# Kernel optimization log

Measured on AMD Instinct MI355X. Metric: run time of the kernel, lower is better.

The kernel has to match this reference:

```python
import jax, jax.numpy as jnp
import numpy as np

N_NODES = 100000
N_EDGES = 1600000
IN_CH = 128
HEADS = 4
OUT_CH = 32


def setup_inputs() -> dict:
    key = jax.random.key(0)
    k = jax.random.split(key, 6)
    x = jax.random.normal(k[0], (N_NODES, IN_CH), dtype=jnp.float32)
    edge_index = jax.random.randint(k[1], (2, N_EDGES), 0, N_NODES, dtype=jnp.int64)
    edge_weight = jax.random.uniform(k[2], (N_EDGES,), dtype=jnp.float32)
    # torch Linear weight layout: (out_features, in_features) = (heads*out_ch, in_ch)
    W = jax.random.normal(k[3], (HEADS * OUT_CH, IN_CH), dtype=jnp.float32) * (1.0 / np.sqrt(IN_CH))
    a_src = jax.random.normal(k[4], (1, HEADS, OUT_CH), dtype=jnp.float32) * 0.1
    a_dst = jax.random.normal(k[5], (1, HEADS, OUT_CH), dtype=jnp.float32) * 0.1
    return {"x": x, "edge_index": edge_index, "edge_weight": edge_weight,
            "W": W, "a_src": a_src, "a_dst": a_dst}


def reference(x, edge_index, edge_weight, W, a_src, a_dst):
    N = x.shape[0]
    H, C = a_src.shape[1], a_src.shape[2]
    # linear projection then reshape to (N, H, C)
    h = (x @ W.T).reshape(N, H, C)
    src, dst = edge_index[0], edge_index[1]
    # per-node attention logits (node-level, then gathered -> same math as
    # (h[src]*a_src).sum(-1), computed once per node instead of per edge)
    s_src = jnp.sum(h * a_src, axis=-1)  # (N, H)
    s_dst = jnp.sum(h * a_dst, axis=-1)  # (N, H)
    alpha = jax.nn.leaky_relu(s_src[src] + s_dst[dst], negative_slope=0.2)  # (E, H)
    alpha = alpha * edge_weight[:, None]
    # segment softmax over dst; torch scatter_reduce amax with include_self=True
    # includes the zero init, so max is taken vs. 0 via zeros init
    amax = jnp.zeros((N, H), dtype=alpha.dtype).at[dst].max(alpha)
    alpha = jnp.exp(alpha - amax[dst])
    asum = jnp.zeros((N, H), dtype=alpha.dtype).at[dst].add(alpha)
    alpha = alpha / (asum[dst] + 1e-8)  # (E, H)
    # weighted scatter-add aggregation
    out = jnp.zeros((N, H, C), dtype=h.dtype).at[dst].add(h[src] * alpha[:, :, None])
    # concat=True
    return out.reshape(N, H * C)
```

## Files before the change

### kernel.cpp

```cpp
#include <hip/hip_runtime.h>

#define N_NODES 100000
#define N_EDGES 1600000
#define NBKT 391
#define BKT_SLACK 5120
#define EPB 4096
#define BINA_BLOCKS ((N_EDGES + EPB - 1) / EPB)

typedef __attribute__((ext_vector_type(8))) short short8;
typedef __attribute__((ext_vector_type(4))) float f32x4;

__device__ __forceinline__ unsigned short f2bf(float f) {
    unsigned u = __float_as_uint(f);
    u = u + 0x7fffu + ((u >> 16) & 1u);
    return (unsigned short)(u >> 16);
}
__device__ __forceinline__ float bf2f(unsigned short h) {
    return __uint_as_float((unsigned)h << 16);
}

__global__ __launch_bounds__(256) void proj_kernel(
    const float* __restrict__ x, const float* __restrict__ W,
    const float* __restrict__ a_src, const float* __restrict__ a_dst,
    unsigned short* __restrict__ hout, float* __restrict__ s_src,
    float* __restrict__ s_dst)
{
    __shared__ char smem[81920];
    char* Wh = smem;
    char* Wl = smem + 32768;
    char* xh = smem + 65536;
    char* xl = smem + 73728;
    const int t = threadIdx.x;
    const int br = blockIdx.x * 32;

    {
        int o = t >> 1, kh = (t & 1) * 64;
#pragma unroll
        for (int i = 0; i < 16; ++i) {
            int k = kh + i * 4;
            float4 v = *(const float4*)&W[o * 128 + k];
            ushort4 hi, lo;
            hi.x = f2bf(v.x); lo.x = f2bf(v.x - bf2f(hi.x));
            hi.y = f2bf(v.y); lo.y = f2bf(v.y - bf2f(hi.y));
            hi.z = f2bf(v.z); lo.z = f2bf(v.z - bf2f(hi.z));
            hi.w = f2bf(v.w); lo.w = f2bf(v.w - bf2f(hi.w));
            int byt = o * 256 + (((k >> 3) ^ (o & 7)) * 16) + (k & 7) * 2;
            *(ushort4*)(Wh + byt) = hi;
            *(ushort4*)(Wl + byt) = lo;
        }
    }
    {
        int row = t >> 3;
        size_t gb = (size_t)(br + row) * 128;
#pragma unroll
        for (int i = 0; i < 4; ++i) {
            int k = ((t & 7) * 4 + i) * 4;
            float4 v = *(const float4*)&x[gb + k];
            ushort4 hi, lo;
            hi.x = f2bf(v.x); lo.x = f2bf(v.x - bf2f(hi.x));
            hi.y = f2bf(v.y); lo.y = f2bf(v.y - bf2f(hi.y));
            hi.z = f2bf(v.z); lo.z = f2bf(v.z - bf2f(hi.z));
            hi.w = f2bf(v.w); lo.w = f2bf(v.w - bf2f(hi.w));
            int byt = row * 256 + (((k >> 3) ^ (row & 7)) * 16) + (k & 7) * 2;
            *(ushort4*)(xh + byt) = hi;
            *(ushort4*)(xl + byt) = lo;
        }
    }
    __syncthreads();

    const int wave = t >> 6, lane = t & 63;
    const int lr = lane & 15, q = lane >> 4;
    f32x4 acc[2][2] = {};

#pragma unroll
    for (int ks = 0; ks < 4; ++ks) {
        int sl = ((ks * 4 + q) ^ (lr & 7)) * 16;
        int a0o = lr * 256 + sl, a1o = (16 + lr) * 256 + sl;
        int b0o = (wave * 32 + lr) * 256 + sl, b1o = (wave * 32 + 16 + lr) * 256 + sl;
        short8 ah0 = *(const short8*)(xh + a0o);
        short8 ah1 = *(const short8*)(xh + a1o);
        short8 al0 = *(const short8*)(xl + a0o);
        short8 al1 = *(const short8*)(xl + a1o);
        short8 bh0 = *(const short8*)(Wh + b0o);
        short8 bh1 = *(const short8*)(Wh + b1o);
        short8 bl0 = *(const short8*)(Wl + b0o);
        short8 bl1 = *(const short8*)(Wl + b1o);
        acc[0][0] = __builtin_amdgcn_mfma_f32_16x16x32_bf16(ah0, bh0, acc[0][0], 0, 0, 0);
        acc[0][1] = __builtin_amdgcn_mfma_f32_16x16x32_bf16(ah0, bh1, acc[0][1], 0, 0, 0);
        acc[1][0] = __builtin_amdgcn_mfma_f32_16x16x32_bf16(ah1, bh0, acc[1][0], 0, 0, 0);
        acc[1][1] = __builtin_amdgcn_mfma_f32_16x16x32_bf16(ah1, bh1, acc[1][1], 0, 0, 0);
        acc[0][0] = __builtin_amdgcn_mfma_f32_16x16x32_bf16(al0, bh0, acc[0][0], 0, 0, 0);
        acc[0][1] = __builtin_amdgcn_mfma_f32_16x16x32_bf16(al0, bh1, acc[0][1], 0, 0, 0);
        acc[1][0] = __builtin_amdgcn_mfma_f32_16x16x32_bf16(al1, bh0, acc[1][0], 0, 0, 0);
        acc[1][1] = __builtin_amdgcn_mfma_f32_16x16x32_bf16(al1, bh1, acc[1][1], 0, 0, 0);
        acc[0][0] = __builtin_amdgcn_mfma_f32_16x16x32_bf16(ah0, bl0, acc[0][0], 0, 0, 0);
        acc[0][1] = __builtin_amdgcn_mfma_f32_16x16x32_bf16(ah0, bl1, acc[0][1], 0, 0, 0);
        acc[1][0] = __builtin_amdgcn_mfma_f32_16x16x32_bf16(ah1, bl0, acc[1][0], 0, 0, 0);
        acc[1][1] = __builtin_amdgcn_mfma_f32_16x16x32_bf16(ah1, bl1, acc[1][1], 0, 0, 0);
    }

    float as0 = a_src[wave * 32 + lr], as1 = a_src[wave * 32 + 16 + lr];
    float ad0 = a_dst[wave * 32 + lr], ad1 = a_dst[wave * 32 + 16 + lr];
#pragma unroll
    for (int r = 0; r < 2; ++r) {
#pragma unroll
        for (int reg = 0; reg < 4; ++reg) {
            float ps = acc[r][0][reg] * as0 + acc[r][1][reg] * as1;
            float pd = acc[r][0][reg] * ad0 + acc[r][1][reg] * ad1;
            ps += __shfl_xor(ps, 1); ps += __shfl_xor(ps, 2);
            ps += __shfl_xor(ps, 4); ps += __shfl_xor(ps, 8);
            pd += __shfl_xor(pd, 1); pd += __shfl_xor(pd, 2);
            pd += __shfl_xor(pd, 4); pd += __shfl_xor(pd, 8);
            if (lr == 0) {
                int grow = br + r * 16 + q * 4 + reg;
                s_src[grow * 4 + wave] = ps;
                s_dst[grow * 4 + wave] = pd;
            }
        }
    }

    __syncthreads();
    unsigned short* hl = (unsigned short*)xh;
#pragma unroll
    for (int r = 0; r < 2; ++r)
#pragma unroll
        for (int c = 0; c < 2; ++c)
#pragma unroll
            for (int reg = 0; reg < 4; ++reg)
                hl[(r * 16 + q * 4 + reg) * 128 + wave * 32 + c * 16 + lr] =
                    f2bf(acc[r][c][reg]);
    __syncthreads();
    {
        int row = t >> 3, cb = (t & 7) * 16;
        uint4 v0 = *(uint4*)&hl[row * 128 + cb];
        uint4 v1 = *(uint4*)&hl[row * 128 + cb + 8];
        *(uint4*)&hout[(size_t)(br + row) * 128 + cb] = v0;
        *(uint4*)&hout[(size_t)(br + row) * 128 + cb + 8] = v1;
    }
}

__global__ __launch_bounds__(256) void binA_kernel(
    const int* __restrict__ ei, const float* __restrict__ ew,
    int* __restrict__ gcur, uint2* __restrict__ ebin)
{
    __shared__ int hist[NBKT];
    __shared__ int runbase[NBKT];
    const int t = threadIdx.x;
    const int base = blockIdx.x * EPB;
    for (int b = t; b < NBKT; b += 256) hist[b] = 0;
    __syncthreads();
#pragma unroll
    for (int i = 0; i < EPB / 256; ++i) {
        int e = base + i * 256 + t;
        if (e < N_EDGES) atomicAdd(&hist[ei[N_EDGES + e] >> 8], 1);
    }
    __syncthreads();
    for (int b = t; b < NBKT; b += 256) {
        int c = hist[b];
        runbase[b] = (c > 0) ? atomicAdd(&gcur[b], c) : 0;
        hist[b] = 0;
    }
    __syncthreads();
#pragma unroll
    for (int i = 0; i < EPB / 256; ++i) {
        int e = base + i * 256 + t;
        if (e >= N_EDGES) continue;
        int s = ei[e];
        int d = ei[N_EDGES + e];
        int b = d >> 8;
        int lpos = atomicAdd(&hist[b], 1);
        ebin[(size_t)b * BKT_SLACK + runbase[b] + lpos] =
            make_uint2((unsigned)s | ((unsigned)(d & 255) << 17),
                       __float_as_uint(ew[e]));
    }
}

__global__ __launch_bounds__(256) void binB_kernel(
    const uint2* __restrict__ ebin, const int* __restrict__ gcur,
    uint2* __restrict__ earr, int* __restrict__ rowp, int* __restrict__ deg)
{
    __shared__ int cnt[256];
    __shared__ int sc[256];
    __shared__ int cur[256];
    const int b = blockIdx.x;
    const int t = threadIdx.x;
    int acc = 0;
    for (int i = t; i < b; i += 256) acc += gcur[i];
    sc[t] = acc; __syncthreads();
    for (int off = 1; off < 256; off <<= 1) {
        int a = sc[t];
        int bb = (t >= off) ? sc[t - off] : 0;
        __syncthreads();
        sc[t] = a + bb;
        __syncthreads();
    }
    const int base = sc[255];
    __syncthreads();
    cnt[t] = 0;
    __syncthreads();
    const int count = gcur[b];
    const uint2* bp = ebin + (size_t)b * BKT_SLACK;
    for (int i = t; i < count; i += 256)
        atomicAdd(&cnt[(bp[i].x >> 17) & 255], 1);
    __syncthreads();
    int c = cnt[t];
    sc[t] = c; __syncthreads();
    for (int off = 1; off < 256; off <<= 1) {
        int a = sc[t];
        int bb = (t >= off) ? sc[t - off] : 0;
        __syncthreads();
        sc[t] = a + bb;
        __syncthreads();
    }
    int excl = sc[t] - c;
    int node = b * 256 + t;
    if (node < N_NODES) { rowp[node] = base + excl; deg[node] = c; }
    cur[t] = base + excl;
    __syncthreads();
    for (int i = t; i < count; i += 256) {
        uint2 rec = bp[i];
        int pos = atomicAdd(&cur[(rec.x >> 17) & 255], 1);
        earr[pos] = make_uint2(rec.x & 0x1FFFFu, rec.y);
    }
}

__global__ __launch_bounds__(256) void gather_kernel(
    const uint2* __restrict__ earr, const int* __restrict__ rowp,
    const int* __restrict__ deg, const float* __restrict__ s_src,
    const float* __restrict__ s_dst,
    const unsigned short* __restrict__ hbuf, float* __restrict__ out)
{
    __shared__ float lds_alpha[16][16][4];
    __shared__ int lds_src[16][16];
    const int ln = threadIdx.x >> 4;
    const int sub = threadIdx.x & 15;
    const int n = blockIdx.x * 16 + ln;
    const int start = rowp[n];
    const int dg = deg[n];
    const float4 sd = *(const float4*)&s_dst[n * 4];
    const int hd3 = sub >> 2;

    float ps0 = 0.f, ps1 = 0.f, ps2 = 0.f, ps3 = 0.f;
    float ac0 = 0.f, ac1 = 0.f, ac2 = 0.f, ac3 = 0.f;
    float ac4 = 0.f, ac5 = 0.f, ac6 = 0.f, ac7 = 0.f;

    for (int b0 = 0; b0 < dg; b0 += 16) {
        int nb = dg - b0; if (nb > 16) nb = 16;
        float a0 = 0.f, a1 = 0.f, a2 = 0.f, a3 = 0.f;
        int sid = 0;
        if (sub < nb) {
            uint2 rec = earr[start + b0 + sub];
            sid = (int)rec.x;
            float wgt = __uint_as_float(rec.y);
            float4 ss = *(const float4*)&s_src[sid * 4];
            float v;
            v = ss.x + sd.x; v = (v > 0.f ? v : 0.2f * v) * wgt; a0 = __expf(v);
            v = ss.y + sd.y; v = (v > 0.f ? v : 0.2f * v) * wgt; a1 = __expf(v);
            v = ss.z + sd.z; v = (v > 0.f ? v : 0.2f * v) * wgt; a2 = __expf(v);
            v = ss.w + sd.w; v = (v > 0.f ? v : 0.2f * v) * wgt; a3 = __expf(v);
            ps0 += a0; ps1 += a1; ps2 += a2; ps3 += a3;
        }
        *(float4*)&lds_alpha[ln][sub][0] = make_float4(a0, a1, a2, a3);
        lds_src[ln][sub] = sid;

#pragma unroll 2
        for (int e = 0; e < nb; ++e) {
            float coef = lds_alpha[ln][e][hd3];
            int s = lds_src[ln][e];
            uint4 hv = *(const uint4*)&hbuf[(size_t)s * 128 + sub * 8];
            ac0 = fmaf(coef, __uint_as_float(hv.x << 16), ac0);
            ac1 = fmaf(coef, __uint_as_float(hv.x & 0xffff0000u), ac1);
            ac2 = fmaf(coef, __uint_as_float(hv.y << 16), ac2);
            ac3 = fmaf(coef, __uint_as_float(hv.y & 0xffff0000u), ac3);
            ac4 = fmaf(coef, __uint_as_float(hv.z << 16), ac4);
            ac5 = fmaf(coef, __uint_as_float(hv.z & 0xffff0000u), ac5);
            ac6 = fmaf(coef, __uint_as_float(hv.w << 16), ac6);
            ac7 = fmaf(coef, __uint_as_float(hv.w & 0xffff0000u), ac7);
        }
    }
#pragma unroll
    for (int off = 1; off < 16; off <<= 1) {
        ps0 += __shfl_xor(ps0, off);
        ps1 += __shfl_xor(ps1, off);
        ps2 += __shfl_xor(ps2, off);
        ps3 += __shfl_xor(ps3, off);
    }
    float sv = (hd3 & 2) ? ((hd3 & 1) ? ps3 : ps2) : ((hd3 & 1) ? ps1 : ps0);
    float inv = 1.f / (sv + 1e-8f);
    float4 o0 = {ac0 * inv, ac1 * inv, ac2 * inv, ac3 * inv};
    float4 o1 = {ac4 * inv, ac5 * inv, ac6 * inv, ac7 * inv};
    *(float4*)&out[(size_t)n * 128 + sub * 8] = o0;
    *(float4*)&out[(size_t)n * 128 + sub * 8 + 4] = o1;
}

extern "C" void kernel_launch(void* const* d_in, const int* in_sizes, int n_in,
                              void* d_out, int out_size, void* d_ws, size_t ws_size,
                              hipStream_t stream)
{
    const float* x     = (const float*)d_in[0];
    const int*   ei    = (const int*)d_in[1];
    const float* ew    = (const float*)d_in[2];
    const float* W     = (const float*)d_in[3];
    const float* a_src = (const float*)d_in[4];
    const float* a_dst = (const float*)d_in[5];
    float* out = (float*)d_out;
    char* ws = (char*)d_ws;

    unsigned short* hbuf = (unsigned short*)(ws);
    float* s_src = (float*)(ws + 25600000);
    float* s_dst = (float*)(ws + 27200000);
    int*   deg   = (int*)(ws + 28800000);
    int*   rowp  = (int*)(ws + 29200000);
    int*   gcur  = (int*)(ws + 29600000);
    uint2* earr  = (uint2*)(ws + 29669632);
    uint2* ebin  = (uint2*)(ws + 42469632);

    hipMemsetAsync(gcur, 0, 2048, stream);

    proj_kernel<<<N_NODES / 32, 256, 0, stream>>>(x, W, a_src, a_dst,
                                                  hbuf, s_src, s_dst);
    binA_kernel<<<BINA_BLOCKS, 256, 0, stream>>>(ei, ew, gcur, ebin);
    binB_kernel<<<NBKT, 256, 0, stream>>>(ebin, gcur, earr, rowp, deg);
    gather_kernel<<<N_NODES / 16, 256, 0, stream>>>(earr, rowp, deg, s_src, s_dst,
                                                    hbuf, out);
}
```

Baseline: 179.8 us.

## Keep projection weights in registers and batch gather loads per 16-edge chunk

The projection kernel now loads each wave's slice of W directly into registers as bf16 hi/lo fragments instead of staging the whole matrix in shared memory. This cuts LDS use from 80KB to 16KB, which raises achievable occupancy. The gather kernel issues all 16 neighbour-row loads for a chunk before doing any FMAs, giving more memory-level parallelism. Inactive slots have zero coefficients and read row 0 harmlessly, but the full 16 loads run even for partial chunks. The LDS arrays are also padded to 17 entries per node.

```diff
diff --git a/kernel.cpp b/kernel.cpp
--- a/kernel.cpp
+++ b/kernel.cpp
@@ -25,30 +25,36 @@
     unsigned short* __restrict__ hout, float* __restrict__ s_src,
     float* __restrict__ s_dst)
 {
-    __shared__ char smem[81920];
-    char* Wh = smem;
-    char* Wl = smem + 32768;
-    char* xh = smem + 65536;
-    char* xl = smem + 73728;
+    __shared__ char smem[16384];
+    char* xh = smem;
+    char* xl = smem + 8192;
     const int t = threadIdx.x;
     const int br = blockIdx.x * 32;
-
-    {
-        int o = t >> 1, kh = (t & 1) * 64;
-#pragma unroll
-        for (int i = 0; i < 16; ++i) {
-            int k = kh + i * 4;
-            float4 v = *(const float4*)&W[o * 128 + k];
-            ushort4 hi, lo;
-            hi.x = f2bf(v.x); lo.x = f2bf(v.x - bf2f(hi.x));
-            hi.y = f2bf(v.y); lo.y = f2bf(v.y - bf2f(hi.y));
-            hi.z = f2bf(v.z); lo.z = f2bf(v.z - bf2f(hi.z));
-            hi.w = f2bf(v.w); lo.w = f2bf(v.w - bf2f(hi.w));
-            int byt = o * 256 + (((k >> 3) ^ (o & 7)) * 16) + (k & 7) * 2;
-            *(ushort4*)(Wh + byt) = hi;
-            *(ushort4*)(Wl + byt) = lo;
-        }
-    }
+    const int wave = t >> 6, lane = t & 63;
+    const int lr = lane & 15, q = lane >> 4;
+
+    short8 wh[2][4], wl[2][4];
+#pragma unroll
+    for (int ct = 0; ct < 2; ++ct) {
+#pragma unroll
+        for (int ks = 0; ks < 4; ++ks) {
+            int o = wave * 32 + ct * 16 + lr;
+            int k0 = (ks * 4 + q) * 8;
+            float4 v0 = *(const float4*)&W[o * 128 + k0];
+            float4 v1 = *(const float4*)&W[o * 128 + k0 + 4];
+            float vv[8] = {v0.x, v0.y, v0.z, v0.w, v1.x, v1.y, v1.z, v1.w};
+            short8 h8, l8;
+#pragma unroll
+            for (int j = 0; j < 8; ++j) {
+                unsigned short hi = f2bf(vv[j]);
+                h8[j] = (short)hi;
+                l8[j] = (short)f2bf(vv[j] - bf2f(hi));
+            }
+            wh[ct][ks] = h8;
+            wl[ct][ks] = l8;
+        }
+    }
+
     {
         int row = t >> 3;
         size_t gb = (size_t)(br + row) * 128;
@@ -68,35 +74,28 @@
     }
     __syncthreads();
 
-    const int wave = t >> 6, lane = t & 63;
-    const int lr = lane & 15, q = lane >> 4;
     f32x4 acc[2][2] = {};
 
 #pragma unroll
     for (int ks = 0; ks < 4; ++ks) {
         int sl = ((ks * 4 + q) ^ (lr & 7)) * 16;
         int a0o = lr * 256 + sl, a1o = (16 + lr) * 256 + sl;
-        int b0o = (wave * 32 + lr) * 256 + sl, b1o = (wave * 32 + 16 + lr) * 256 + sl;
         short8 ah0 = *(const short8*)(xh + a0o);
         short8 ah1 = *(const short8*)(xh + a1o);
         short8 al0 = *(const short8*)(xl + a0o);
         short8 al1 = *(const short8*)(xl + a1o);
-        short8 bh0 = *(const short8*)(Wh + b0o);
-        short8 bh1 = *(const short8*)(Wh + b1o);
-        short8 bl0 = *(const short8*)(Wl + b0o);
-        short8 bl1 = *(const short8*)(Wl + b1o);
-        acc[0][0] = __builtin_amdgcn_mfma_f32_16x16x32_bf16(ah0, bh0, acc[0][0], 0, 0, 0);
-        acc[0][1] = __builtin_amdgcn_mfma_f32_16x16x32_bf16(ah0, bh1, acc[0][1], 0, 0, 0);
-        acc[1][0] = __builtin_amdgcn_mfma_f32_16x16x32_bf16(ah1, bh0, acc[1][0], 0, 0, 0);
-        acc[1][1] = __builtin_amdgcn_mfma_f32_16x16x32_bf16(ah1, bh1, acc[1][1], 0, 0, 0);
-        acc[0][0] = __builtin_amdgcn_mfma_f32_16x16x32_bf16(al0, bh0, acc[0][0], 0, 0, 0);
-        acc[0][1] = __builtin_amdgcn_mfma_f32_16x16x32_bf16(al0, bh1, acc[0][1], 0, 0, 0);
-        acc[1][0] = __builtin_amdgcn_mfma_f32_16x16x32_bf16(al1, bh0, acc[1][0], 0, 0, 0);
-        acc[1][1] = __builtin_amdgcn_mfma_f32_16x16x32_bf16(al1, bh1, acc[1][1], 0, 0, 0);
-        acc[0][0] = __builtin_amdgcn_mfma_f32_16x16x32_bf16(ah0, bl0, acc[0][0], 0, 0, 0);
-        acc[0][1] = __builtin_amdgcn_mfma_f32_16x16x32_bf16(ah0, bl1, acc[0][1], 0, 0, 0);
-        acc[1][0] = __builtin_amdgcn_mfma_f32_16x16x32_bf16(ah1, bl0, acc[1][0], 0, 0, 0);
-        acc[1][1] = __builtin_amdgcn_mfma_f32_16x16x32_bf16(ah1, bl1, acc[1][1], 0, 0, 0);
+        acc[0][0] = __builtin_amdgcn_mfma_f32_16x16x32_bf16(ah0, wh[0][ks], acc[0][0], 0, 0, 0);
+        acc[0][1] = __builtin_amdgcn_mfma_f32_16x16x32_bf16(ah0, wh[1][ks], acc[0][1], 0, 0, 0);
+        acc[1][0] = __builtin_amdgcn_mfma_f32_16x16x32_bf16(ah1, wh[0][ks], acc[1][0], 0, 0, 0);
+        acc[1][1] = __builtin_amdgcn_mfma_f32_16x16x32_bf16(ah1, wh[1][ks], acc[1][1], 0, 0, 0);
+        acc[0][0] = __builtin_amdgcn_mfma_f32_16x16x32_bf16(al0, wh[0][ks], acc[0][0], 0, 0, 0);
+        acc[0][1] = __builtin_amdgcn_mfma_f32_16x16x32_bf16(al0, wh[1][ks], acc[0][1], 0, 0, 0);
+        acc[1][0] = __builtin_amdgcn_mfma_f32_16x16x32_bf16(al1, wh[0][ks], acc[1][0], 0, 0, 0);
+        acc[1][1] = __builtin_amdgcn_mfma_f32_16x16x32_bf16(al1, wh[1][ks], acc[1][1], 0, 0, 0);
+        acc[0][0] = __builtin_amdgcn_mfma_f32_16x16x32_bf16(ah0, wl[0][ks], acc[0][0], 0, 0, 0);
+        acc[0][1] = __builtin_amdgcn_mfma_f32_16x16x32_bf16(ah0, wl[1][ks], acc[0][1], 0, 0, 0);
+        acc[1][0] = __builtin_amdgcn_mfma_f32_16x16x32_bf16(ah1, wl[0][ks], acc[1][0], 0, 0, 0);
+        acc[1][1] = __builtin_amdgcn_mfma_f32_16x16x32_bf16(ah1, wl[1][ks], acc[1][1], 0, 0, 0);
     }
 
     float as0 = a_src[wave * 32 + lr], as1 = a_src[wave * 32 + 16 + lr];
@@ -120,7 +119,7 @@
     }
 
     __syncthreads();
-    unsigned short* hl = (unsigned short*)xh;
+    unsigned short* hl = (unsigned short*)smem;
 #pragma unroll
     for (int r = 0; r < 2; ++r)
 #pragma unroll
@@ -230,8 +229,8 @@
     const float* __restrict__ s_dst,
     const unsigned short* __restrict__ hbuf, float* __restrict__ out)
 {
-    __shared__ float lds_alpha[16][16][4];
-    __shared__ int lds_src[16][16];
+    __shared__ float lds_alpha[16][17][4];
+    __shared__ int lds_src[16][17];
     const int ln = threadIdx.x >> 4;
     const int sub = threadIdx.x & 15;
     const int n = blockIdx.x * 16 + ln;
@@ -263,19 +262,24 @@
         *(float4*)&lds_alpha[ln][sub][0] = make_float4(a0, a1, a2, a3);
         lds_src[ln][sub] = sid;
 
-#pragma unroll 2
-        for (int e = 0; e < nb; ++e) {
-            float coef = lds_alpha[ln][e][hd3];
+        float co[16];
+        uint4 hv[16];
+#pragma unroll
+        for (int e = 0; e < 16; ++e) {
+            co[e] = lds_alpha[ln][e][hd3];
             int s = lds_src[ln][e];
-            uint4 hv = *(const uint4*)&hbuf[(size_t)s * 128 + sub * 8];
-            ac0 = fmaf(coef, __uint_as_float(hv.x << 16), ac0);
-            ac1 = fmaf(coef, __uint_as_float(hv.x & 0xffff0000u), ac1);
-            ac2 = fmaf(coef, __uint_as_float(hv.y << 16), ac2);
-            ac3 = fmaf(coef, __uint_as_float(hv.y & 0xffff0000u), ac3);
-            ac4 = fmaf(coef, __uint_as_float(hv.z << 16), ac4);
-            ac5 = fmaf(coef, __uint_as_float(hv.z & 0xffff0000u), ac5);
-            ac6 = fmaf(coef, __uint_as_float(hv.w << 16), ac6);
-            ac7 = fmaf(coef, __uint_as_float(hv.w & 0xffff0000u), ac7);
+            hv[e] = *(const uint4*)&hbuf[(size_t)s * 128 + sub * 8];
+        }
+#pragma unroll
+        for (int e = 0; e < 16; ++e) {
+            ac0 = fmaf(co[e], __uint_as_float(hv[e].x << 16), ac0);
+            ac1 = fmaf(co[e], __uint_as_float(hv[e].x & 0xffff0000u), ac1);
+            ac2 = fmaf(co[e], __uint_as_float(hv[e].y << 16), ac2);
+            ac3 = fmaf(co[e], __uint_as_float(hv[e].y & 0xffff0000u), ac3);
+            ac4 = fmaf(co[e], __uint_as_float(hv[e].z << 16), ac4);
+            ac5 = fmaf(co[e], __uint_as_float(hv[e].z & 0xffff0000u), ac5);
+            ac6 = fmaf(co[e], __uint_as_float(hv[e].w << 16), ac6);
+            ac7 = fmaf(co[e], __uint_as_float(hv[e].w & 0xffff0000u), ac7);
         }
     }
 #pragma unroll
```

After: 166.0 us. -7.7%, faster.
